# Kernel tuning notes

Hardware: AMD Instinct MI355X
Metric: run time of the kernel (lower is better)

Reference implementation:

```python
import jax, jax.numpy as jnp
import numpy as np


def setup_inputs() -> dict:
    key = jax.random.key(0)
    k1, k2 = jax.random.split(key)
    x = jax.random.normal(k1, (8, 2500, 100), dtype=jnp.float32)          # [B, L, E]
    label_feature = jax.random.normal(k2, (8922, 100), dtype=jnp.float32)  # [N, E]
    return {"x": x, "label_feature": label_feature}


def reference(x, label_feature):
    # scores: [B, N, L] = label_feature @ x^T (broadcast query over batch), unscaled
    scores = jnp.einsum("ne,ble->bnl", label_feature, x)
    alpha = jax.nn.softmax(scores, axis=2)  # softmax over sequence length
    # m: [B, N, E] = alpha @ x
    m = jnp.einsum("bnl,ble->bne", alpha, x)
    return m
```

## Files before the change

### kernel.cpp

```cpp
#include <hip/hip_runtime.h>
#include <math.h>
#include <stdint.h>

typedef __attribute__((ext_vector_type(8))) _Float16 half8;
typedef __attribute__((ext_vector_type(4))) _Float16 half4;
typedef __attribute__((ext_vector_type(4))) float f32x4;

constexpr int Bb = 8, Ll = 2500, Ee = 100, Nn = 8922;
constexpr int LP = 2560, EP = 128, NP = 8960;
constexpr int LT = 32;
constexpr int NTILES = LP / LT;
constexpr int NTB = 128;

constexpr size_t SZ_LF = (size_t)NP * EP * 2;
constexpr size_t SZ_XW = (size_t)Bb * LP * EP * 2;
constexpr size_t OFF_XW = SZ_LF;
constexpr size_t OFF_XT = OFF_XW + SZ_XW;
constexpr size_t WS_NEED = OFF_XT + SZ_XW;

__device__ __forceinline__ void gload16(const void* g, void* l) {
    __builtin_amdgcn_global_load_lds(
        (const __attribute__((address_space(1))) uint32_t*)g,
        (__attribute__((address_space(3))) uint32_t*)l, 16, 0, 0);
}

__global__ __launch_bounds__(256)
void prep_lf(const float* __restrict__ lf, uint32_t* __restrict__ dst) {
    int idx = blockIdx.x * 256 + threadIdx.x;
    int n = idx >> 6, ep = idx & 63;
    int e0 = 2 * ep, e1 = e0 + 1;
    float f0 = (n < Nn && e0 < Ee) ? lf[(size_t)n * Ee + e0] : 0.f;
    float f1 = (n < Nn && e1 < Ee) ? lf[(size_t)n * Ee + e1] : (e1 == 127 ? 1.0f : 0.f);
    union { _Float16 h[2]; uint32_t u; } cv;
    cv.h[0] = (_Float16)f0; cv.h[1] = (_Float16)f1;
    dst[idx] = cv.u;
}

__global__ __launch_bounds__(256)
void prep_x(const float* __restrict__ x, uint32_t* __restrict__ dxw,
            uint16_t* __restrict__ dxt) {
    __shared__ float lx[64][101];
    const int l0 = blockIdx.x * 64;
    const int b  = blockIdx.y;
    for (int i = threadIdx.x; i < 64 * Ee; i += 256) {
        int ll = i / Ee, e = i - ll * Ee;
        int l = l0 + ll;
        lx[ll][e] = (l < Ll) ? x[((size_t)b * Ll + l) * Ee + e] : 0.f;
    }
    __syncthreads();
    for (int i = threadIdx.x; i < 64 * 64; i += 256) {
        int row = i >> 6, ep = i & 63;
        int l = l0 + row;
        int e0 = 2 * ep, e1 = e0 + 1;
        float f0 = (e0 < Ee) ? lx[row][e0] : 0.f;
        float f1;
        if (e1 < Ee)        f1 = lx[row][e1];
        else if (e1 == 127) f1 = (l < Ll) ? 0.f : -20000.f;
        else                f1 = 0.f;
        union { _Float16 h[2]; uint32_t u; } cv;
        cv.h[0] = (_Float16)f0; cv.h[1] = (_Float16)f1;
        int boff = (4 * ep) ^ ((row & 7) << 4);
        dxw[((size_t)b * LP + l) * 64 + (boff >> 2)] = cv.u;
    }
    for (int i = threadIdx.x; i < EP * 64; i += 256) {
        int e = i >> 6, ll = i & 63;
        float v = (e < Ee) ? lx[ll][e] : 0.f;
        uint32_t boff = (uint32_t)((2 * ll) ^ ((e & 3) << 4));
        union { _Float16 h; uint16_t u; } cv; cv.h = (_Float16)v;
        dxt[((size_t)b * EP + e) * LP + l0 + (boff >> 1)] = cv.u;
    }
}

__global__ __launch_bounds__(256, 4)
void cwa_mfma(const uint16_t* __restrict__ lf16, const uint16_t* __restrict__ xw,
              const uint16_t* __restrict__ xt, float* __restrict__ out) {
    __shared__ __align__(128) char smem[16384 + 16384 + 8192];
    const int tid = threadIdx.x, lane = tid & 63, w = tid >> 6;
    const int g = lane >> 4, nl = lane & 15;
    const int b = blockIdx.y;
    const int n_base = blockIdx.x * NTB + w * 32;

    half8 qf[2][4];
#pragma unroll
    for (int nh = 0; nh < 2; nh++) {
        const uint16_t* qr = lf16 + (size_t)(n_base + 16 * nh + nl) * EP + 8 * g;
#pragma unroll
        for (int ks = 0; ks < 4; ks++) qf[nh][ks] = *(const half8*)(qr + 32 * ks);
    }

    f32x4 oacc[2][7];
#pragma unroll
    for (int nh = 0; nh < 2; nh++)
#pragma unroll
        for (int es = 0; es < 7; es++) oacc[nh][es] = f32x4{0.f, 0.f, 0.f, 0.f};
    float m_i[2] = {-INFINITY, -INFINITY}, s_i[2] = {0.f, 0.f};

    const char* xwb = (const char*)(xw + (size_t)b * LP * EP);
    const char* xtb = (const char*)(xt + (size_t)b * EP * LP);

    auto stage = [&](int t, int par) {
        char* kbuf = smem + par * 8192;
        char* vbuf = smem + 16384 + par * 8192;
        const char* kg = xwb + (size_t)t * LT * EP * 2;
        const char* vg = xtb + (size_t)t * LT * 2;
#pragma unroll
        for (int i = 0; i < 2; i++) {
            int off = i * 4096 + w * 1024 + lane * 16;
            gload16(kg + off, kbuf + off);
        }
#pragma unroll
        for (int i = 0; i < 2; i++) {
            int erow = i * 64 + w * 16 + (lane >> 2);
            gload16(vg + (size_t)erow * (LP * 2) + (lane & 3) * 16,
                    vbuf + i * 4096 + w * 1024 + lane * 16);
        }
    };

    stage(0, 0);
    asm volatile("s_waitcnt vmcnt(0)" ::: "memory");
    __syncthreads();

    char* pb = smem + 32768 + w * 2048;
    const int swp = (nl & 3) << 4;

    for (int t = 0; t < NTILES; t++) {
        const int par = t & 1;
        const char* kb = smem + par * 8192;
        const char* vb = smem + 16384 + par * 8192;

        if (t + 1 < NTILES) stage(t + 1, par ^ 1);

        f32x4 sacc[2][2];
#pragma unroll
        for (int nh = 0; nh < 2; nh++)
#pragma unroll
            for (int ls = 0; ls < 2; ls++) sacc[nh][ls] = f32x4{0.f, 0.f, 0.f, 0.f};
#pragma unroll
        for (int ls = 0; ls < 2; ls++) {
            const int lrow = 16 * ls + nl;
            const char* kr = kb + lrow * 256;
            const int sw = (lrow & 7) << 4;
#pragma unroll
            for (int ks = 0; ks < 4; ks++) {
                half8 kf = *(const half8*)(kr + ((64 * ks + 16 * g) ^ sw));
                sacc[0][ls] = __builtin_amdgcn_mfma_f32_16x16x32_f16(kf, qf[0][ks], sacc[0][ls], 0, 0, 0);
                sacc[1][ls] = __builtin_amdgcn_mfma_f32_16x16x32_f16(kf, qf[1][ks], sacc[1][ls], 0, 0, 0);
            }
        }

        float tm[2];
#pragma unroll
        for (int nh = 0; nh < 2; nh++) {
            float a0 = fmaxf(fmaxf(sacc[nh][0][0], sacc[nh][0][1]),
                             fmaxf(sacc[nh][0][2], sacc[nh][0][3]));
            float a1 = fmaxf(fmaxf(sacc[nh][1][0], sacc[nh][1][1]),
                             fmaxf(sacc[nh][1][2], sacc[nh][1][3]));
            float tmv = fmaxf(a0, a1);
            tmv = fmaxf(tmv, __shfl_xor(tmv, 16, 64));
            tmv = fmaxf(tmv, __shfl_xor(tmv, 32, 64));
            tm[nh] = tmv;
        }

        if (!__all((tm[0] <= m_i[0] + 8.f) && (tm[1] <= m_i[1] + 8.f))) {
#pragma unroll
            for (int nh = 0; nh < 2; nh++) {
                const float mn = fmaxf(m_i[nh], tm[nh]);
                const float sc = __expf(m_i[nh] - mn);
                m_i[nh] = mn;
                s_i[nh] *= sc;
#pragma unroll
                for (int r = 0; r < 4; r++) {
                    float scr = __shfl(sc, 4 * g + r, 64);
#pragma unroll
                    for (int es = 0; es < 7; es++) oacc[nh][es][r] *= scr;
                }
            }
        }

#pragma unroll
        for (int nh = 0; nh < 2; nh++) {
            float ts = 0.f;
            half4 ph[2];
#pragma unroll
            for (int ls = 0; ls < 2; ls++)
#pragma unroll
                for (int r = 0; r < 4; r++) {
                    float pv = __expf(sacc[nh][ls][r] - m_i[nh]);
                    ts += pv;
                    ph[ls][r] = (_Float16)pv;
                }
            ts += __shfl_xor(ts, 16, 64);
            ts += __shfl_xor(ts, 32, 64);
            s_i[nh] += ts;
#pragma unroll
            for (int ls = 0; ls < 2; ls++)
                *(half4*)(pb + (16 * nh + nl) * 64 + ((32 * ls + 8 * g) ^ swp)) = ph[ls];
        }

        {
            half8 pf0 = *(const half8*)(pb + nl * 64 + ((16 * g) ^ swp));
            half8 pf1 = *(const half8*)(pb + (16 + nl) * 64 + ((16 * g) ^ swp));
#pragma unroll
            for (int es = 0; es < 7; es++) {
                const int er = 16 * es + nl;
                half8 vf = *(const half8*)(vb + er * 64 + ((16 * g) ^ ((er & 3) << 4)));
                oacc[0][es] = __builtin_amdgcn_mfma_f32_16x16x32_f16(pf0, vf, oacc[0][es], 0, 0, 0);
                oacc[1][es] = __builtin_amdgcn_mfma_f32_16x16x32_f16(pf1, vf, oacc[1][es], 0, 0, 0);
            }
        }

        asm volatile("s_waitcnt vmcnt(0)" ::: "memory");
        __syncthreads();
    }

#pragma unroll
    for (int nh = 0; nh < 2; nh++) {
        const float inv = 1.0f / s_i[nh];
#pragma unroll
        for (int r = 0; r < 4; r++) {
            const float invr = __shfl(inv, 4 * g + r, 64);
            const int n = n_base + 16 * nh + 4 * g + r;
            if (n < Nn) {
#pragma unroll
                for (int es = 0; es < 7; es++) {
                    const int e = 16 * es + nl;
                    if (e < Ee) out[((size_t)b * Nn + n) * Ee + e] = oacc[nh][es][r] * invr;
                }
            }
        }
    }
}

constexpr int FNT = 16, FLT = 64, FLTP = 65;
__global__ __launch_bounds__(256)
void cwa_fwd(const float* __restrict__ x, const float* __restrict__ lf,
             float* __restrict__ out) {
    __shared__ float q[FNT][Ee];
    __shared__ float xts[Ee][FLTP];
    __shared__ float pl[FNT][FLT];
    const int tid = threadIdx.x, lane = tid & 63, w = tid >> 6;
    const int b = blockIdx.y, n0 = blockIdx.x * FNT;
    for (int idx = tid; idx < FNT * Ee; idx += 256) {
        int nl = idx / Ee, e = idx - nl * Ee;
        int n = n0 + nl;
        q[nl][e] = (n < Nn) ? lf[n * Ee + e] : 0.0f;
    }
    float m_i[4], s_i[4], a0[4], a1[4];
#pragma unroll
    for (int i = 0; i < 4; i++) { m_i[i] = -INFINITY; s_i[i] = 0.f; a0[i] = 0.f; a1[i] = 0.f; }
    const float* xb = x + (size_t)b * Ll * Ee;
    const bool hi_ok = lane < (Ee - 64);
    for (int l0 = 0; l0 < Ll; l0 += FLT) {
        const int nrows = min(FLT, Ll - l0);
        __syncthreads();
        for (int idx = tid; idx < FLT * (Ee / 4); idx += 256) {
            int r = idx / (Ee / 4), c4 = idx - r * (Ee / 4);
            float4 v = make_float4(0.f, 0.f, 0.f, 0.f);
            if (r < nrows) v = *reinterpret_cast<const float4*>(xb + (size_t)(l0 + r) * Ee + c4 * 4);
            xts[c4 * 4 + 0][r] = v.x; xts[c4 * 4 + 1][r] = v.y;
            xts[c4 * 4 + 2][r] = v.z; xts[c4 * 4 + 3][r] = v.w;
        }
        __syncthreads();
        float sc[4] = {0.f, 0.f, 0.f, 0.f};
        for (int e = 0; e < Ee; e++) {
            float xv = xts[e][lane];
#pragma unroll
            for (int i = 0; i < 4; i++) sc[i] = fmaf(q[4 * w + i][e], xv, sc[i]);
        }
        const bool valid = lane < nrows;
#pragma unroll
        for (int i = 0; i < 4; i++) {
            float s = valid ? sc[i] : -INFINITY;
            float tmv = s;
#pragma unroll
            for (int msk = 32; msk >= 1; msk >>= 1) tmv = fmaxf(tmv, __shfl_xor(tmv, msk, 64));
            float mn = fmaxf(m_i[i], tmv);
            float p = __expf(s - mn);
            float sm = p;
#pragma unroll
            for (int msk = 32; msk >= 1; msk >>= 1) sm += __shfl_xor(sm, msk, 64);
            float scl = __expf(m_i[i] - mn);
            s_i[i] = s_i[i] * scl + sm; m_i[i] = mn;
            a0[i] *= scl; a1[i] *= scl;
            pl[4 * w + i][lane] = p;
        }
        __syncthreads();
#pragma unroll 4
        for (int l = 0; l < FLT; l++) {
            float xv0 = xts[lane][l];
            float xv1 = hi_ok ? xts[64 + lane][l] : 0.f;
#pragma unroll
            for (int i = 0; i < 4; i++) {
                float pv = pl[4 * w + i][l];
                a0[i] = fmaf(pv, xv0, a0[i]); a1[i] = fmaf(pv, xv1, a1[i]);
            }
        }
    }
#pragma unroll
    for (int i = 0; i < 4; i++) {
        int n = n0 + 4 * w + i;
        if (n >= Nn) continue;
        float inv = 1.0f / s_i[i];
        size_t base = ((size_t)b * Nn + n) * Ee;
        out[base + lane] = a0[i] * inv;
        if (hi_ok) out[base + 64 + lane] = a1[i] * inv;
    }
}

extern "C" void kernel_launch(void* const* d_in, const int* in_sizes, int n_in,
                              void* d_out, int out_size, void* d_ws, size_t ws_size,
                              hipStream_t stream) {
    const float* x  = (const float*)d_in[0];
    const float* lf = (const float*)d_in[1];
    float* out = (float*)d_out;
    if (ws_size >= WS_NEED) {
        prep_lf<<<NP * 64 / 256, 256, 0, stream>>>(lf, (uint32_t*)d_ws);
        prep_x<<<dim3(LP / 64, Bb), 256, 0, stream>>>(
            x, (uint32_t*)((char*)d_ws + OFF_XW), (uint16_t*)((char*)d_ws + OFF_XT));
        cwa_mfma<<<dim3(NP / NTB, Bb), 256, 0, stream>>>(
            (const uint16_t*)d_ws, (const uint16_t*)((char*)d_ws + OFF_XW),
            (const uint16_t*)((char*)d_ws + OFF_XT), out);
    } else {
        dim3 grid((Nn + FNT - 1) / FNT, Bb);
        cwa_fwd<<<grid, dim3(256), 0, stream>>>(x, lf, out);
    }
}
```

Measured before the change: 292.8 us.

## Enlarge attention tiles to 64 keys and 48 queries per wave, merge prep kernels

Each wave now handles three 16-row query groups and each step covers 64 sequence positions, so every K/V tile loaded into LDS feeds more MFMA work. The V transpose is trimmed from 128 to 112 embedding rows, which cuts global and LDS traffic. K is double-buffered and V single-buffered, with a revised wait/barrier schedule. The two prep kernels are merged into one launch. In exchange, occupancy drops to 2 blocks per CU because of higher register and LDS use, and the last N tile gets more padding.

```diff
diff --git a/kernel.cpp b/kernel.cpp
--- a/kernel.cpp
+++ b/kernel.cpp
@@ -7,16 +7,20 @@
 typedef __attribute__((ext_vector_type(4))) float f32x4;
 
 constexpr int Bb = 8, Ll = 2500, Ee = 100, Nn = 8922;
-constexpr int LP = 2560, EP = 128, NP = 8960;
-constexpr int LT = 32;
+constexpr int LP = 2560, EP = 128;
+constexpr int NP = 9024;
+constexpr int VE = 112;
+constexpr int LT = 64;
 constexpr int NTILES = LP / LT;
-constexpr int NTB = 128;
+constexpr int NTB = 192;
+constexpr int NH = 3;
 
 constexpr size_t SZ_LF = (size_t)NP * EP * 2;
 constexpr size_t SZ_XW = (size_t)Bb * LP * EP * 2;
+constexpr size_t SZ_XT = (size_t)Bb * VE * LP * 2;
 constexpr size_t OFF_XW = SZ_LF;
 constexpr size_t OFF_XT = OFF_XW + SZ_XW;
-constexpr size_t WS_NEED = OFF_XT + SZ_XW;
+constexpr size_t WS_NEED = OFF_XT + SZ_XT;
 
 __device__ __forceinline__ void gload16(const void* g, void* l) {
     __builtin_amdgcn_global_load_lds(
@@ -25,20 +29,21 @@
 }
 
 __global__ __launch_bounds__(256)
-void prep_lf(const float* __restrict__ lf, uint32_t* __restrict__ dst) {
-    int idx = blockIdx.x * 256 + threadIdx.x;
-    int n = idx >> 6, ep = idx & 63;
-    int e0 = 2 * ep, e1 = e0 + 1;
-    float f0 = (n < Nn && e0 < Ee) ? lf[(size_t)n * Ee + e0] : 0.f;
-    float f1 = (n < Nn && e1 < Ee) ? lf[(size_t)n * Ee + e1] : (e1 == 127 ? 1.0f : 0.f);
-    union { _Float16 h[2]; uint32_t u; } cv;
-    cv.h[0] = (_Float16)f0; cv.h[1] = (_Float16)f1;
-    dst[idx] = cv.u;
-}
-
-__global__ __launch_bounds__(256)
-void prep_x(const float* __restrict__ x, uint32_t* __restrict__ dxw,
-            uint16_t* __restrict__ dxt) {
+void prep_all(const float* __restrict__ x, const float* __restrict__ lf,
+              uint32_t* __restrict__ dlf, uint32_t* __restrict__ dxw,
+              uint16_t* __restrict__ dxt) {
+    if (blockIdx.y == Bb) {
+        for (int idx = blockIdx.x * 256 + threadIdx.x; idx < NP * 64; idx += 40 * 256) {
+            int n = idx >> 6, ep = idx & 63;
+            int e0 = 2 * ep, e1 = e0 + 1;
+            float f0 = (n < Nn && e0 < Ee) ? lf[(size_t)n * Ee + e0] : 0.f;
+            float f1 = (n < Nn && e1 < Ee) ? lf[(size_t)n * Ee + e1] : (e1 == 127 ? 1.0f : 0.f);
+            union { _Float16 h[2]; uint32_t u; } cv;
+            cv.h[0] = (_Float16)f0; cv.h[1] = (_Float16)f1;
+            dlf[idx] = cv.u;
+        }
+        return;
+    }
     __shared__ float lx[64][101];
     const int l0 = blockIdx.x * 64;
     const int b  = blockIdx.y;
@@ -62,81 +67,86 @@
         int boff = (4 * ep) ^ ((row & 7) << 4);
         dxw[((size_t)b * LP + l) * 64 + (boff >> 2)] = cv.u;
     }
-    for (int i = threadIdx.x; i < EP * 64; i += 256) {
+    for (int i = threadIdx.x; i < VE * 64; i += 256) {
         int e = i >> 6, ll = i & 63;
         float v = (e < Ee) ? lx[ll][e] : 0.f;
-        uint32_t boff = (uint32_t)((2 * ll) ^ ((e & 3) << 4));
+        uint32_t boff = (uint32_t)((2 * ll) ^ ((e & 7) << 4));
         union { _Float16 h; uint16_t u; } cv; cv.h = (_Float16)v;
-        dxt[((size_t)b * EP + e) * LP + l0 + (boff >> 1)] = cv.u;
-    }
-}
-
-__global__ __launch_bounds__(256, 4)
+        dxt[((size_t)b * VE + e) * LP + l0 + (boff >> 1)] = cv.u;
+    }
+}
+
+__global__ __launch_bounds__(256, 2)
 void cwa_mfma(const uint16_t* __restrict__ lf16, const uint16_t* __restrict__ xw,
               const uint16_t* __restrict__ xt, float* __restrict__ out) {
-    __shared__ __align__(128) char smem[16384 + 16384 + 8192];
+    __shared__ __align__(128) char smem[71680];
     const int tid = threadIdx.x, lane = tid & 63, w = tid >> 6;
     const int g = lane >> 4, nl = lane & 15;
     const int b = blockIdx.y;
-    const int n_base = blockIdx.x * NTB + w * 32;
-
-    half8 qf[2][4];
-#pragma unroll
-    for (int nh = 0; nh < 2; nh++) {
+    const int n_base = blockIdx.x * NTB + w * 48;
+
+    const char* xwb = (const char*)(xw + (size_t)b * LP * EP);
+    const char* xtb = (const char*)(xt + (size_t)b * VE * LP);
+
+    auto stage_k = [&](int t, int p) {
+        const char* kg = xwb + (size_t)t * (LT * EP * 2);
+        char* kbuf = smem + p * 16384;
+#pragma unroll
+        for (int i = 0; i < 4; i++) {
+            int off = i * 4096 + tid * 16;
+            gload16(kg + off, kbuf + off);
+        }
+    };
+    auto stage_v = [&](int t) {
+        const char* vg = xtb + (size_t)t * (LT * 2);
+        char* vbuf = smem + 32768;
+#pragma unroll
+        for (int i = 0; i < 3; i++) {
+            int u = i * 256 + tid;
+            gload16(vg + (size_t)(u >> 3) * (LP * 2) + (u & 7) * 16, vbuf + u * 16);
+        }
+        if (tid < 128) {
+            int u = 768 + tid;
+            gload16(vg + (size_t)(u >> 3) * (LP * 2) + (u & 7) * 16, vbuf + u * 16);
+        }
+    };
+
+    stage_k(0, 0);
+    stage_v(0);
+
+    half8 qf[NH][4];
+#pragma unroll
+    for (int nh = 0; nh < NH; nh++) {
         const uint16_t* qr = lf16 + (size_t)(n_base + 16 * nh + nl) * EP + 8 * g;
 #pragma unroll
         for (int ks = 0; ks < 4; ks++) qf[nh][ks] = *(const half8*)(qr + 32 * ks);
     }
-
-    f32x4 oacc[2][7];
-#pragma unroll
-    for (int nh = 0; nh < 2; nh++)
-#pragma unroll
-        for (int es = 0; es < 7; es++) oacc[nh][es] = f32x4{0.f, 0.f, 0.f, 0.f};
-    float m_i[2] = {-INFINITY, -INFINITY}, s_i[2] = {0.f, 0.f};
-
-    const char* xwb = (const char*)(xw + (size_t)b * LP * EP);
-    const char* xtb = (const char*)(xt + (size_t)b * EP * LP);
-
-    auto stage = [&](int t, int par) {
-        char* kbuf = smem + par * 8192;
-        char* vbuf = smem + 16384 + par * 8192;
-        const char* kg = xwb + (size_t)t * LT * EP * 2;
-        const char* vg = xtb + (size_t)t * LT * 2;
-#pragma unroll
-        for (int i = 0; i < 2; i++) {
-            int off = i * 4096 + w * 1024 + lane * 16;
-            gload16(kg + off, kbuf + off);
-        }
-#pragma unroll
-        for (int i = 0; i < 2; i++) {
-            int erow = i * 64 + w * 16 + (lane >> 2);
-            gload16(vg + (size_t)erow * (LP * 2) + (lane & 3) * 16,
-                    vbuf + i * 4096 + w * 1024 + lane * 16);
-        }
-    };
-
-    stage(0, 0);
     asm volatile("s_waitcnt vmcnt(0)" ::: "memory");
     __syncthreads();
-
-    char* pb = smem + 32768 + w * 2048;
-    const int swp = (nl & 3) << 4;
+    stage_k(1, 1);
+
+    f32x4 oacc[NH][7];
+#pragma unroll
+    for (int nh = 0; nh < NH; nh++)
+#pragma unroll
+        for (int es = 0; es < 7; es++) oacc[nh][es] = f32x4{0.f, 0.f, 0.f, 0.f};
+    float m_i[NH] = {-INFINITY, -INFINITY, -INFINITY}, s_i[NH] = {0.f, 0.f, 0.f};
+
+    const char* vb = smem + 32768;
+    char* pb = smem + 47104 + w * 6144;
+    const int swp = (nl & 7) << 4;
 
     for (int t = 0; t < NTILES; t++) {
-        const int par = t & 1;
-        const char* kb = smem + par * 8192;
-        const char* vb = smem + 16384 + par * 8192;
-
-        if (t + 1 < NTILES) stage(t + 1, par ^ 1);
-
-        f32x4 sacc[2][2];
-#pragma unroll
-        for (int nh = 0; nh < 2; nh++)
-#pragma unroll
-            for (int ls = 0; ls < 2; ls++) sacc[nh][ls] = f32x4{0.f, 0.f, 0.f, 0.f};
-#pragma unroll
-        for (int ls = 0; ls < 2; ls++) {
+        const int p = t & 1;
+        const char* kb = smem + p * 16384;
+
+        f32x4 sacc[NH][4];
+#pragma unroll
+        for (int nh = 0; nh < NH; nh++)
+#pragma unroll
+            for (int ls = 0; ls < 4; ls++) sacc[nh][ls] = f32x4{0.f, 0.f, 0.f, 0.f};
+#pragma unroll
+        for (int ls = 0; ls < 4; ls++) {
             const int lrow = 16 * ls + nl;
             const char* kr = kb + lrow * 256;
             const int sw = (lrow & 7) << 4;
@@ -145,25 +155,26 @@
                 half8 kf = *(const half8*)(kr + ((64 * ks + 16 * g) ^ sw));
                 sacc[0][ls] = __builtin_amdgcn_mfma_f32_16x16x32_f16(kf, qf[0][ks], sacc[0][ls], 0, 0, 0);
                 sacc[1][ls] = __builtin_amdgcn_mfma_f32_16x16x32_f16(kf, qf[1][ks], sacc[1][ls], 0, 0, 0);
-            }
-        }
-
-        float tm[2];
-#pragma unroll
-        for (int nh = 0; nh < 2; nh++) {
-            float a0 = fmaxf(fmaxf(sacc[nh][0][0], sacc[nh][0][1]),
-                             fmaxf(sacc[nh][0][2], sacc[nh][0][3]));
-            float a1 = fmaxf(fmaxf(sacc[nh][1][0], sacc[nh][1][1]),
-                             fmaxf(sacc[nh][1][2], sacc[nh][1][3]));
-            float tmv = fmaxf(a0, a1);
+                sacc[2][ls] = __builtin_amdgcn_mfma_f32_16x16x32_f16(kf, qf[2][ks], sacc[2][ls], 0, 0, 0);
+            }
+        }
+
+        float tm[NH];
+#pragma unroll
+        for (int nh = 0; nh < NH; nh++) {
+            float a0 = fmaxf(fmaxf(sacc[nh][0][0], sacc[nh][0][1]), fmaxf(sacc[nh][0][2], sacc[nh][0][3]));
+            float a1 = fmaxf(fmaxf(sacc[nh][1][0], sacc[nh][1][1]), fmaxf(sacc[nh][1][2], sacc[nh][1][3]));
+            float a2 = fmaxf(fmaxf(sacc[nh][2][0], sacc[nh][2][1]), fmaxf(sacc[nh][2][2], sacc[nh][2][3]));
+            float a3 = fmaxf(fmaxf(sacc[nh][3][0], sacc[nh][3][1]), fmaxf(sacc[nh][3][2], sacc[nh][3][3]));
+            float tmv = fmaxf(fmaxf(a0, a1), fmaxf(a2, a3));
             tmv = fmaxf(tmv, __shfl_xor(tmv, 16, 64));
             tmv = fmaxf(tmv, __shfl_xor(tmv, 32, 64));
             tm[nh] = tmv;
         }
 
-        if (!__all((tm[0] <= m_i[0] + 8.f) && (tm[1] <= m_i[1] + 8.f))) {
-#pragma unroll
-            for (int nh = 0; nh < 2; nh++) {
+        if (!__all((tm[0] <= m_i[0] + 8.f) && (tm[1] <= m_i[1] + 8.f) && (tm[2] <= m_i[2] + 8.f))) {
+#pragma unroll
+            for (int nh = 0; nh < NH; nh++) {
                 const float mn = fmaxf(m_i[nh], tm[nh]);
                 const float sc = __expf(m_i[nh] - mn);
                 m_i[nh] = mn;
@@ -178,11 +189,11 @@
         }
 
 #pragma unroll
-        for (int nh = 0; nh < 2; nh++) {
+        for (int nh = 0; nh < NH; nh++) {
             float ts = 0.f;
-            half4 ph[2];
-#pragma unroll
-            for (int ls = 0; ls < 2; ls++)
+            half4 ph[4];
+#pragma unroll
+            for (int ls = 0; ls < 4; ls++)
 #pragma unroll
                 for (int r = 0; r < 4; r++) {
                     float pv = __expf(sacc[nh][ls][r] - m_i[nh]);
@@ -193,28 +204,36 @@
             ts += __shfl_xor(ts, 32, 64);
             s_i[nh] += ts;
 #pragma unroll
-            for (int ls = 0; ls < 2; ls++)
-                *(half4*)(pb + (16 * nh + nl) * 64 + ((32 * ls + 8 * g) ^ swp)) = ph[ls];
-        }
-
-        {
-            half8 pf0 = *(const half8*)(pb + nl * 64 + ((16 * g) ^ swp));
-            half8 pf1 = *(const half8*)(pb + (16 + nl) * 64 + ((16 * g) ^ swp));
+            for (int ls = 0; ls < 4; ls++)
+                *(half4*)(pb + (16 * nh + nl) * 128 + ((32 * ls + 8 * g) ^ swp)) = ph[ls];
+        }
+
+#pragma unroll
+        for (int kl = 0; kl < 2; kl++) {
+            half8 pf0 = *(const half8*)(pb + nl * 128 + ((64 * kl + 16 * g) ^ swp));
+            half8 pf1 = *(const half8*)(pb + (16 + nl) * 128 + ((64 * kl + 16 * g) ^ swp));
+            half8 pf2 = *(const half8*)(pb + (32 + nl) * 128 + ((64 * kl + 16 * g) ^ swp));
 #pragma unroll
             for (int es = 0; es < 7; es++) {
                 const int er = 16 * es + nl;
-                half8 vf = *(const half8*)(vb + er * 64 + ((16 * g) ^ ((er & 3) << 4)));
+                half8 vf = *(const half8*)(vb + er * 128 + ((64 * kl + 16 * g) ^ ((er & 7) << 4)));
                 oacc[0][es] = __builtin_amdgcn_mfma_f32_16x16x32_f16(pf0, vf, oacc[0][es], 0, 0, 0);
                 oacc[1][es] = __builtin_amdgcn_mfma_f32_16x16x32_f16(pf1, vf, oacc[1][es], 0, 0, 0);
-            }
-        }
-
-        asm volatile("s_waitcnt vmcnt(0)" ::: "memory");
-        __syncthreads();
-    }
-
-#pragma unroll
-    for (int nh = 0; nh < 2; nh++) {
+                oacc[2][es] = __builtin_amdgcn_mfma_f32_16x16x32_f16(pf2, vf, oacc[2][es], 0, 0, 0);
+            }
+        }
+
+        __syncthreads();
+        const int tv = min(t + 1, NTILES - 1);
+        const int tk = min(t + 2, NTILES - 1);
+        stage_v(tv);
+        stage_k(tk, p);
+        asm volatile("s_waitcnt vmcnt(4)" ::: "memory");
+        __syncthreads();
+    }
+
+#pragma unroll
+    for (int nh = 0; nh < NH; nh++) {
         const float inv = 1.0f / s_i[nh];
 #pragma unroll
         for (int r = 0; r < 4; r++) {
@@ -275,14 +294,14 @@
 #pragma unroll
             for (int msk = 32; msk >= 1; msk >>= 1) tmv = fmaxf(tmv, __shfl_xor(tmv, msk, 64));
             float mn = fmaxf(m_i[i], tmv);
-            float p = __expf(s - mn);
-            float sm = p;
+            float pp = __expf(s - mn);
+            float sm = pp;
 #pragma unroll
             for (int msk = 32; msk >= 1; msk >>= 1) sm += __shfl_xor(sm, msk, 64);
             float scl = __expf(m_i[i] - mn);
             s_i[i] = s_i[i] * scl + sm; m_i[i] = mn;
             a0[i] *= scl; a1[i] *= scl;
-            pl[4 * w + i][lane] = p;
+            pl[4 * w + i][lane] = pp;
         }
         __syncthreads();
 #pragma unroll 4
@@ -314,12 +333,12 @@
     const float* lf = (const float*)d_in[1];
     float* out = (float*)d_out;
     if (ws_size >= WS_NEED) {
-        prep_lf<<<NP * 64 / 256, 256, 0, stream>>>(lf, (uint32_t*)d_ws);
-        prep_x<<<dim3(LP / 64, Bb), 256, 0, stream>>>(
-            x, (uint32_t*)((char*)d_ws + OFF_XW), (uint16_t*)((char*)d_ws + OFF_XT));
+        uint32_t* dlf = (uint32_t*)d_ws;
+        uint32_t* dxw = (uint32_t*)((char*)d_ws + OFF_XW);
+        uint16_t* dxt = (uint16_t*)((char*)d_ws + OFF_XT);
+        prep_all<<<dim3(LP / 64, Bb + 1), 256, 0, stream>>>(x, lf, dlf, dxw, dxt);
         cwa_mfma<<<dim3(NP / NTB, Bb), 256, 0, stream>>>(
-            (const uint16_t*)d_ws, (const uint16_t*)((char*)d_ws + OFF_XW),
-            (const uint16_t*)((char*)d_ws + OFF_XT), out);
+            (const uint16_t*)dlf, (const uint16_t*)dxw, dxt, out);
     } else {
         dim3 grid((Nn + FNT - 1) / FNT, Bb);
         cwa_fwd<<<grid, dim3(256), 0, stream>>>(x, lf, out);
```

Result: faster. 238.6 us (-18.5%).
